# Kernel tuning notes

Hardware: AMD Instinct MI355X
Metric: run time of the kernel (lower is better)

Reference implementation:

```python
import jax, jax.numpy as jnp
import numpy as np

B, S, D, H, F, NL, V = 4, 2048, 512, 8, 2048, 4, 32000
DH = D // H
EPS = 1e-6
LN_EPS = 1e-5


def _xavier(k, shape):
    lim = (6.0 / (shape[-2] + shape[-1])) ** 0.5
    return jax.random.uniform(k, shape, jnp.float32, -lim, lim)


def setup_inputs() -> dict:
    key = jax.random.key(0)
    ks = jax.random.split(key, 12)
    x = jax.random.randint(ks[0], (B, S), 0, V)
    emb = jax.random.normal(ks[1], (V, D), jnp.float32) * 0.02
    # sinusoidal positional encoding
    pos = np.arange(S, dtype=np.float32)[:, None]
    div = np.exp(np.arange(0, D, 2, dtype=np.float32) * (-np.log(10000.0) / D))
    pe_np = np.zeros((S, D), np.float32)
    pe_np[:, 0::2] = np.sin(pos * div)
    pe_np[:, 1::2] = np.cos(pos * div)
    pe = jnp.asarray(pe_np)
    return {
        "x": x, "emb": emb, "pe": pe,
        "Wq": _xavier(ks[2], (NL, D, D)), "bq": jnp.zeros((NL, D)),
        "Wk": _xavier(ks[3], (NL, D, D)), "bk": jnp.zeros((NL, D)),
        "Wv": _xavier(ks[4], (NL, D, D)), "bv": jnp.zeros((NL, D)),
        "Wo": _xavier(ks[5], (NL, D, D)), "bo": jnp.zeros((NL, D)),
        "W1": _xavier(ks[6], (NL, D, F)), "b1": jnp.zeros((NL, F)),
        "W2": _xavier(ks[7], (NL, F, D)), "b2": jnp.zeros((NL, D)),
        "g1": jnp.ones((NL, D)), "be1": jnp.zeros((NL, D)),
        "g2": jnp.ones((NL, D)), "be2": jnp.zeros((NL, D)),
        "gf": jnp.ones((D,)), "bf": jnp.zeros((D,)),
    }


def _layer_norm(h, g, b):
    mu = jnp.mean(h, axis=-1, keepdims=True)
    var = jnp.mean((h - mu) ** 2, axis=-1, keepdims=True)
    return (h - mu) * jax.lax.rsqrt(var + LN_EPS) * g + b


def _phi(u):
    # elu(x) + 1 feature map of fast-transformers causal-linear attention
    return jax.nn.elu(u) + 1.0


def _causal_linear_attention(q, k, v, key_mask):
    # q, k, v: [B, S, H, DH]; key_mask: [B, S] (1 for valid keys)
    Q = _phi(q)
    K = _phi(k) * key_mask[:, :, None, None]
    # cumulative state sum_{j<=i} K_j outer V_j : [B, S, H, DH, DH]
    St = jnp.cumsum(K[..., :, None] * v[..., None, :], axis=1)
    num = jnp.einsum("bshd,bshde->bshe", Q, St)
    Z = 1.0 / (jnp.einsum("bshd,bshd->bsh", Q, jnp.cumsum(K, axis=1)) + EPS)
    return num * Z[..., None]


def reference(x, emb, pe, Wq, bq, Wk, bk, Wv, bv, Wo, bo,
              W1, b1, W2, b2, g1, be1, g2, be2, gf, bf):
    # length mask from nonzero token count (LengthMask semantics)
    lengths = jnp.sum(jnp.abs(x) != 0, axis=-1)  # [B]
    key_mask = (jnp.arange(S)[None, :] < lengths[:, None]).astype(jnp.float32)
    h = emb[x] + pe[None, :, :]  # [B, S, D]
    for i in range(NL):
        q = (h @ Wq[i] + bq[i]).reshape(B, S, H, DH)
        k = (h @ Wk[i] + bk[i]).reshape(B, S, H, DH)
        v = (h @ Wv[i] + bv[i]).reshape(B, S, H, DH)
        a = _causal_linear_attention(q, k, v, key_mask).reshape(B, S, D)
        a = a @ Wo[i] + bo[i]
        h = _layer_norm(h + a, g1[i], be1[i])
        y = jax.nn.relu(h @ W1[i] + b1[i]) @ W2[i] + b2[i]
        h = _layer_norm(h + y, g2[i], be2[i])
    return _layer_norm(h, gf, bf)
```

## Files before the change

kernel.cpp:

```cpp
#include <hip/hip_runtime.h>
#include <math.h>

#define NLAYER 4
#define BB 4
#define SS 2048
#define DD 512
#define HH 8
#define DH 64
#define FF 2048
#define TT (BB*SS)
#define LCH 64
#define NCH (SS/LCH)
#define LN_EPS 1e-5f
#define ATT_EPS 1e-6f

typedef __bf16 bf16x8 __attribute__((ext_vector_type(8)));
typedef float  f32x4  __attribute__((ext_vector_type(4)));

__device__ __forceinline__ unsigned short f2bf(float f) {
    union { float f; unsigned u; } a; a.f = f;
    unsigned u = a.u;
    unsigned r = (u + 0x7FFFu + ((u >> 16) & 1u)) >> 16;
    return (unsigned short)r;
}
__device__ __forceinline__ float bf2f(unsigned short s) {
    union { unsigned u; float f; } a; a.u = ((unsigned)s) << 16;
    return a.f;
}
__device__ __forceinline__ float phi_f(float u) {
    return u > 0.f ? u + 1.f : __expf(u);
}

__global__ __launch_bounds__(64)
void len_kernel(const int* __restrict__ x, int* __restrict__ len) {
    const int b = blockIdx.x;
    int cnt = 0;
    for (int s = threadIdx.x; s < SS; s += 64) cnt += (x[b * SS + s] != 0);
    #pragma unroll
    for (int off = 32; off; off >>= 1) cnt += __shfl_xor(cnt, off);
    if (threadIdx.x == 0) len[b] = cnt;
}

__global__ __launch_bounds__(256)
void embed_kernel(const int* __restrict__ x, const float* __restrict__ emb,
                  const float* __restrict__ pe, float* __restrict__ h,
                  unsigned short* __restrict__ h_bf) {
    int t = blockIdx.x * 256 + threadIdx.x;
    int row = t >> 7;
    int q = t & 127;
    int tok = x[row];
    int s = row & (SS - 1);
    float4 e = ((const float4*)(emb + (size_t)tok * DD))[q];
    float4 p = ((const float4*)(pe + (size_t)s * DD))[q];
    float4 v; v.x = e.x + p.x; v.y = e.y + p.y; v.z = e.z + p.z; v.w = e.w + p.w;
    ((float4*)(h + (size_t)row * DD))[q] = v;
    ushort4 ub; ub.x = f2bf(v.x); ub.y = f2bf(v.y); ub.z = f2bf(v.z); ub.w = f2bf(v.w);
    ((ushort4*)(h_bf + (size_t)row * DD))[q] = ub;
}

__global__ __launch_bounds__(256)
void transpose_cvt(const float* __restrict__ src, unsigned short* __restrict__ dst,
                   int R, int C, size_t srcLS, size_t dstLS) {
    __shared__ float tile[32][33];
    const int z = blockIdx.z;
    src += (size_t)z * srcLS;
    dst += (size_t)z * dstLS;
    const int c0 = blockIdx.x * 32, r0 = blockIdx.y * 32;
    const int tx = threadIdx.x & 31, ty = threadIdx.x >> 5;
    #pragma unroll
    for (int i = 0; i < 32; i += 8)
        tile[ty + i][tx] = src[(size_t)(r0 + ty + i) * C + c0 + tx];
    __syncthreads();
    #pragma unroll
    for (int i = 0; i < 32; i += 8)
        dst[(size_t)(c0 + ty + i) * R + r0 + tx] = f2bf(tile[tx][ty + i]);
}

__global__ __launch_bounds__(256)
void bias_concat(const float* __restrict__ bq, const float* __restrict__ bk,
                 const float* __restrict__ bv, float* __restrict__ bqkv) {
    int idx = blockIdx.x * 256 + threadIdx.x;
    if (idx >= NLAYER * 1536) return;
    int l = idx / 1536, n = idx % 1536;
    float v = n < 512 ? bq[l * 512 + n] : (n < 1024 ? bk[l * 512 + n - 512] : bv[l * 512 + n - 1024]);
    bqkv[idx] = v;
}

__device__ __forceinline__ void gll16(void* lds_ptr, const void* g_ptr) {
    __builtin_amdgcn_global_load_lds(
        (const __attribute__((address_space(1))) void*)g_ptr,
        (__attribute__((address_space(3))) void*)lds_ptr, 16, 0, 0);
}

template<int RELU, int WF, int WB>
__global__ __launch_bounds__(256, 2)
void gemm_bt(const unsigned short* __restrict__ A, const unsigned short* __restrict__ Bt,
             const float* __restrict__ bias, float* __restrict__ Cf,
             unsigned short* __restrict__ Cb, int M, int N, int K) {
    __shared__ __align__(16) char lds[2 * 2 * 128 * 64 * 2];
    const int Nt = N >> 7;
    const int bid = blockIdx.x;
    const int swz = (bid & 7) * ((int)gridDim.x >> 3) + (bid >> 3);
    const int m0 = (swz / Nt) * 128;
    const int n0 = (swz % Nt) * 128;
    const int tid = threadIdx.x;
    const int w = tid >> 6, lane = tid & 63;
    const int wr = w >> 1, wc = w & 1;
    const int srow = lane >> 3, scc = lane & 7;

    f32x4 acc[4][4] = {};

    auto stage = [&](int buf, int k0) {
        char* base = lds + buf * 32768;
        #pragma unroll
        for (int op = 0; op < 2; ++op) {
            const unsigned short* G = op ? Bt : A;
            const int r0 = op ? n0 : m0;
            char* obase = base + op * 16384;
            #pragma unroll
            for (int i = 0; i < 4; ++i) {
                int ii = w * 4 + i;
                int row = ii * 8 + srow;
                int chunk = scc ^ (row & 7);
                gll16(obase + ii * 1024,
                      G + (size_t)(r0 + row) * K + k0 + chunk * 8);
            }
        }
    };

    stage(0, 0);
    const int nt = K >> 6;
    int buf = 0;
    const int g = lane >> 4;
    const int rA = wr * 64 + (lane & 15);
    const int rB = wc * 64 + (lane & 15);

    for (int kt = 0; kt < nt; ++kt) {
        __syncthreads();
        if (kt + 1 < nt) stage(buf ^ 1, (kt + 1) << 6);
        const char* pA = lds + buf * 32768;
        const char* pB = pA + 16384;
        bf16x8 af[4][2], bfr[4][2];
        #pragma unroll
        for (int m = 0; m < 4; ++m)
            #pragma unroll
            for (int kk = 0; kk < 2; ++kk) {
                int row = rA + m * 16;
                int c = (kk * 4 + g) ^ (row & 7);
                af[m][kk] = *(const bf16x8*)(pA + row * 128 + c * 16);
            }
        #pragma unroll
        for (int n = 0; n < 4; ++n)
            #pragma unroll
            for (int kk = 0; kk < 2; ++kk) {
                int row = rB + n * 16;
                int c = (kk * 4 + g) ^ (row & 7);
                bfr[n][kk] = *(const bf16x8*)(pB + row * 128 + c * 16);
            }
        #pragma unroll
        for (int kk = 0; kk < 2; ++kk)
            #pragma unroll
            for (int m = 0; m < 4; ++m)
                #pragma unroll
                for (int n = 0; n < 4; ++n)
                    acc[m][n] = __builtin_amdgcn_mfma_f32_16x16x32_bf16(
                        af[m][kk], bfr[n][kk], acc[m][n], 0, 0, 0);
        buf ^= 1;
    }

    const int col16 = lane & 15;
    const int rgrp = lane >> 4;
    #pragma unroll
    for (int n = 0; n < 4; ++n) {
        int col = n0 + wc * 64 + n * 16 + col16;
        float bi = bias[col];
        #pragma unroll
        for (int m = 0; m < 4; ++m) {
            int rowb = m0 + wr * 64 + m * 16 + rgrp * 4;
            #pragma unroll
            for (int r = 0; r < 4; ++r) {
                float v = acc[m][n][r] + bi;
                if (RELU) v = v > 0.f ? v : 0.f;
                if (WF) Cf[(size_t)(rowb + r) * N + col] = v;
                if (WB) Cb[(size_t)(rowb + r) * N + col] = f2bf(v);
            }
        }
    }
}

__global__ __launch_bounds__(256)
void attn_chunk_sums(const unsigned short* __restrict__ qkv, const int* __restrict__ len,
                     unsigned short* __restrict__ states, float* __restrict__ ksum) {
    const int c = blockIdx.x & (NCH - 1);
    const int bh = blockIdx.x / NCH;
    const int b = bh >> 3, h = bh & 7;
    const int L = len[b];
    const int tid = threadIdx.x;
    const int w = tid >> 6, lane = tid & 63;
    __shared__ __align__(16) unsigned short Kt[64 * 64];
    __shared__ __align__(16) unsigned short Vt[64 * 64];
    __shared__ float ksumP[4][64];

    float kpart = 0.f;
    #pragma unroll 8
    for (int t = 0; t < 16; ++t) {
        const int jj = 4 * t + w;
        const int d = lane;
        const int sglob = c * 64 + jj;
        const unsigned short* base = qkv + (size_t)(b * SS + sglob) * 1536 + h * 64 + d;
        float kv = bf2f(base[512]);
        float kp = (sglob < L) ? phi_f(kv) : 0.f;
        kpart += kp;
        const int sw = (((jj >> 3) ^ (d & 7)) << 3) + (jj & 7);
        Kt[d * 64 + sw] = f2bf(kp);
        Vt[d * 64 + sw] = base[1024];
    }
    ksumP[w][lane] = kpart;
    __syncthreads();

    const int frow = w * 16 + (lane & 15);
    const int g = lane >> 4;
    bf16x8 ak[2];
    #pragma unroll
    for (int kk = 0; kk < 2; ++kk)
        ak[kk] = *(const bf16x8*)&Kt[frow * 64 + (((kk * 4 + g) ^ (frow & 7)) << 3)];
    f32x4 oc[4] = {};
    #pragma unroll
    for (int ef = 0; ef < 4; ++ef) {
        int brow = ef * 16 + (lane & 15);
        #pragma unroll
        for (int kk = 0; kk < 2; ++kk) {
            bf16x8 bv = *(const bf16x8*)&Vt[brow * 64 + (((kk * 4 + g) ^ (brow & 7)) << 3)];
            oc[ef] = __builtin_amdgcn_mfma_f32_16x16x32_bf16(ak[kk], bv, oc[ef], 0, 0, 0);
        }
    }
    unsigned short* so = states + (size_t)blockIdx.x * 4096;
    #pragma unroll
    for (int ef = 0; ef < 4; ++ef)
        #pragma unroll
        for (int r = 0; r < 4; ++r) {
            int dd = w * 16 + g * 4 + r;
            int e = ef * 16 + (lane & 15);
            so[dd * 64 + e] = f2bf(oc[ef][r]);
        }
    if (w == 0) {
        float s = ksumP[0][lane] + ksumP[1][lane] + ksumP[2][lane] + ksumP[3][lane];
        ksum[(size_t)blockIdx.x * 64 + lane] = s;
    }
}

__global__ __launch_bounds__(256)
void attn_prefix(const unsigned short* __restrict__ states, const float* __restrict__ ksum,
                 unsigned short* __restrict__ sprefix, float* __restrict__ kprefix) {
    const int bh = blockIdx.x >> 4;
    const int idx = (blockIdx.x & 15) * 256 + threadIdx.x;
    size_t base = (size_t)bh * NCH * 4096 + idx;
    float run = 0.f;
    #pragma unroll 4
    for (int cc = 0; cc < NCH; ++cc) {
        size_t o = base + (size_t)cc * 4096;
        float v = bf2f(states[o]);
        sprefix[o] = f2bf(run);
        run += v;
    }
    if ((blockIdx.x & 15) == 0 && threadIdx.x < 64) {
        size_t kb = (size_t)bh * NCH * 64 + threadIdx.x;
        float krun = 0.f;
        for (int cc = 0; cc < NCH; ++cc) {
            size_t o = kb + (size_t)cc * 64;
            float v = ksum[o];
            kprefix[o] = krun;
            krun += v;
        }
    }
}

__global__ __launch_bounds__(256)
void attn_output(const unsigned short* __restrict__ qkv, const int* __restrict__ len,
                 const unsigned short* __restrict__ sprefix, const float* __restrict__ kprefix,
                 unsigned short* __restrict__ a_bf) {
    const int c = blockIdx.x & (NCH - 1);
    const int bh = blockIdx.x / NCH;
    const int b = bh >> 3, h = bh & 7;
    const int L = len[b];
    const int tid = threadIdx.x;
    const int w = tid >> 6, lane = tid & 63;

    __shared__ __align__(16) unsigned short Qb[64 * 64];
    __shared__ __align__(16) unsigned short Kb[64 * 64];
    __shared__ __align__(16) unsigned short SpT[64 * 64];
    __shared__ __align__(16) unsigned short Vt[64 * 64];
    __shared__ __align__(16) unsigned short Amb[64 * 64];
    __shared__ float zq[64];
    __shared__ float zinv[64];

    const float kspv = kprefix[(size_t)(bh * NCH + c) * 64 + lane];
    const unsigned short* Sp = sprefix + (size_t)(bh * NCH + c) * 4096;

    #pragma unroll 4
    for (int t = 0; t < 16; ++t) {
        const int jj = 4 * t + w;
        const int d = lane;
        const int sglob = c * 64 + jj;
        const unsigned short* base = qkv + (size_t)(b * SS + sglob) * 1536 + h * 64 + d;
        float qv = bf2f(base[0]), kv = bf2f(base[512]);
        float qp = phi_f(qv);
        float kp = (sglob < L) ? phi_f(kv) : 0.f;
        const int swr = (((d >> 3) ^ (jj & 7)) << 3) + (d & 7);
        Qb[jj * 64 + swr] = f2bf(qp);
        Kb[jj * 64 + swr] = f2bf(kp);
        const int swt = (((jj >> 3) ^ (d & 7)) << 3) + (jj & 7);
        Vt[d * 64 + swt] = base[1024];
        SpT[d * 64 + swt] = Sp[jj * 64 + d];
        float zc = qp * kspv;
        #pragma unroll
        for (int off = 32; off; off >>= 1) zc += __shfl_xor(zc, off);
        if (lane == 0) zq[jj] = zc;
    }
    __syncthreads();

    const int frow = w * 16 + (lane & 15);
    const int g = lane >> 4;
    bf16x8 aq[2];
    #pragma unroll
    for (int kk = 0; kk < 2; ++kk)
        aq[kk] = *(const bf16x8*)&Qb[frow * 64 + (((kk * 4 + g) ^ (frow & 7)) << 3)];

    f32x4 am[4] = {};
    #pragma unroll
    for (int jf = 0; jf < 4; ++jf) {
        int brow = jf * 16 + (lane & 15);
        #pragma unroll
        for (int kk = 0; kk < 2; ++kk) {
            bf16x8 bk = *(const bf16x8*)&Kb[brow * 64 + (((kk * 4 + g) ^ (brow & 7)) << 3)];
            am[jf] = __builtin_amdgcn_mfma_f32_16x16x32_bf16(aq[kk], bk, am[jf], 0, 0, 0);
        }
    }

    float zl[4] = {0.f, 0.f, 0.f, 0.f};
    #pragma unroll
    for (int jf = 0; jf < 4; ++jf) {
        #pragma unroll
        for (int r = 0; r < 4; ++r) {
            int i = w * 16 + g * 4 + r;
            int j = jf * 16 + (lane & 15);
            float v = (j <= i) ? am[jf][r] : 0.f;
            zl[r] += v;
            Amb[i * 64 + (((j >> 3) ^ (i & 7)) << 3) + (j & 7)] = f2bf(v);
        }
    }
    #pragma unroll
    for (int r = 0; r < 4; ++r)
        #pragma unroll
        for (int off = 1; off < 16; off <<= 1) zl[r] += __shfl_xor(zl[r], off);
    #pragma unroll
    for (int r = 0; r < 4; ++r) {
        if ((lane & 15) == r) {
            int i = w * 16 + g * 4 + r;
            zinv[i] = 1.f / (zl[r] + zq[i] + ATT_EPS);
        }
    }

    f32x4 oc[4] = {};
    #pragma unroll
    for (int ef = 0; ef < 4; ++ef) {
        int brow = ef * 16 + (lane & 15);
        #pragma unroll
        for (int kk = 0; kk < 2; ++kk) {
            bf16x8 bs = *(const bf16x8*)&SpT[brow * 64 + (((kk * 4 + g) ^ (brow & 7)) << 3)];
            oc[ef] = __builtin_amdgcn_mfma_f32_16x16x32_bf16(aq[kk], bs, oc[ef], 0, 0, 0);
        }
    }
    bf16x8 aam[2];
    #pragma unroll
    for (int kk = 0; kk < 2; ++kk)
        aam[kk] = *(const bf16x8*)&Amb[frow * 64 + (((kk * 4 + g) ^ (frow & 7)) << 3)];
    #pragma unroll
    for (int ef = 0; ef < 4; ++ef) {
        int brow = ef * 16 + (lane & 15);
        #pragma unroll
        for (int kk = 0; kk < 2; ++kk) {
            bf16x8 bv = *(const bf16x8*)&Vt[brow * 64 + (((kk * 4 + g) ^ (brow & 7)) << 3)];
            oc[ef] = __builtin_amdgcn_mfma_f32_16x16x32_bf16(aam[kk], bv, oc[ef], 0, 0, 0);
        }
    }

    __syncthreads();
    #pragma unroll
    for (int ef = 0; ef < 4; ++ef) {
        #pragma unroll
        for (int r = 0; r < 4; ++r) {
            int i = w * 16 + g * 4 + r;
            int e = ef * 16 + (lane & 15);
            float zi = zinv[i];
            Kb[i * 64 + (((e >> 3) ^ (i & 7)) << 3) + (e & 7)] = f2bf(oc[ef][r] * zi);
        }
    }
    __syncthreads();
    {
        unsigned short* dst = a_bf + (size_t)(b * SS + c * 64) * 512 + h * 64;
        #pragma unroll
        for (int u = 0; u < 2; ++u) {
            int cid = tid + u * 256;
            int row = cid >> 3, cb = cid & 7;
            int4 val = *(const int4*)&Kb[row * 64 + ((cb ^ (row & 7)) << 3)];
            *(int4*)(dst + (size_t)row * 512 + cb * 8) = val;
        }
    }
}

template<int ADD, int WB>
__global__ __launch_bounds__(64)
void ln_kernel(const float* __restrict__ hin, const float* __restrict__ add,
               const float* __restrict__ gw, const float* __restrict__ bw,
               float* __restrict__ hout, unsigned short* __restrict__ hbf) {
    const int row = blockIdx.x;
    const int lane = threadIdx.x;
    float v[8];
    const float* hp = hin + (size_t)row * DD;
    float s = 0.f;
    #pragma unroll
    for (int i = 0; i < 2; ++i) {
        int q = lane + i * 64;
        float4 a = ((const float4*)hp)[q];
        if (ADD) {
            float4 bb = ((const float4*)(add + (size_t)row * DD))[q];
            a.x += bb.x; a.y += bb.y; a.z += bb.z; a.w += bb.w;
        }
        v[i*4+0] = a.x; v[i*4+1] = a.y; v[i*4+2] = a.z; v[i*4+3] = a.w;
        s += a.x + a.y + a.z + a.w;
    }
    #pragma unroll
    for (int off = 32; off; off >>= 1) s += __shfl_xor(s, off);
    float mu = s * (1.f / 512.f);
    float sq = 0.f;
    #pragma unroll
    for (int i = 0; i < 8; ++i) { float d = v[i] - mu; sq += d * d; }
    #pragma unroll
    for (int off = 32; off; off >>= 1) sq += __shfl_xor(sq, off);
    float rs = 1.f / sqrtf(sq * (1.f / 512.f) + LN_EPS);
    #pragma unroll
    for (int i = 0; i < 2; ++i) {
        int q = lane + i * 64;
        float4 gv = ((const float4*)gw)[q];
        float4 bv = ((const float4*)bw)[q];
        float4 o;
        o.x = (v[i*4+0] - mu) * rs * gv.x + bv.x;
        o.y = (v[i*4+1] - mu) * rs * gv.y + bv.y;
        o.z = (v[i*4+2] - mu) * rs * gv.z + bv.z;
        o.w = (v[i*4+3] - mu) * rs * gv.w + bv.w;
        ((float4*)(hout + (size_t)row * DD))[q] = o;
        if (WB) {
            ushort4 ub; ub.x = f2bf(o.x); ub.y = f2bf(o.y); ub.z = f2bf(o.z); ub.w = f2bf(o.w);
            ((ushort4*)(hbf + (size_t)row * DD))[q] = ub;
        }
    }
}

extern "C" void kernel_launch(void* const* d_in, const int* in_sizes, int n_in,
                              void* d_out, int out_size, void* d_ws, size_t ws_size,
                              hipStream_t stream) {
    (void)in_sizes; (void)n_in; (void)out_size; (void)ws_size;
    const int*   x   = (const int*)d_in[0];
    const float* emb = (const float*)d_in[1];
    const float* pe  = (const float*)d_in[2];
    const float* Wq  = (const float*)d_in[3];
    const float* bq  = (const float*)d_in[4];
    const float* Wk  = (const float*)d_in[5];
    const float* bk  = (const float*)d_in[6];
    const float* Wv  = (const float*)d_in[7];
    const float* bv  = (const float*)d_in[8];
    const float* Wo  = (const float*)d_in[9];
    const float* bo  = (const float*)d_in[10];
    const float* W1  = (const float*)d_in[11];
    const float* b1  = (const float*)d_in[12];
    const float* W2  = (const float*)d_in[13];
    const float* b2  = (const float*)d_in[14];
    const float* g1  = (const float*)d_in[15];
    const float* be1 = (const float*)d_in[16];
    const float* g2  = (const float*)d_in[17];
    const float* be2 = (const float*)d_in[18];
    const float* gf  = (const float*)d_in[19];
    const float* bff = (const float*)d_in[20];
    float* out = (float*)d_out;

    char* ws = (char*)d_ws;
    size_t off = 0;
    auto alloc = [&](size_t bytes) -> void* {
        void* p = ws + off; off += (bytes + 255) & ~(size_t)255; return p;
    };
    int* len              = (int*)alloc(16);
    unsigned short* qkv_t = (unsigned short*)alloc((size_t)NLAYER * 1536 * 512 * 2);
    unsigned short* wo_t  = (unsigned short*)alloc((size_t)NLAYER * 512 * 512 * 2);
    unsigned short* w1_t  = (unsigned short*)alloc((size_t)NLAYER * 2048 * 512 * 2);
    unsigned short* w2_t  = (unsigned short*)alloc((size_t)NLAYER * 512 * 2048 * 2);
    float* bqkv           = (float*)alloc((size_t)NLAYER * 1536 * 4);
    float* h              = (float*)alloc((size_t)TT * 512 * 4);
    unsigned short* h_bf  = (unsigned short*)alloc((size_t)TT * 512 * 2);
    unsigned short* qkv   = (unsigned short*)alloc((size_t)TT * 1536 * 2);
    unsigned short* a_bf  = (unsigned short*)alloc((size_t)TT * 512 * 2);
    float* obuf           = (float*)alloc((size_t)TT * 512 * 4);
    unsigned short* y1_bf = (unsigned short*)alloc((size_t)TT * 2048 * 2);
    unsigned short* states  = (unsigned short*)alloc((size_t)32 * NCH * 4096 * 2);
    float* ksum           = (float*)alloc((size_t)32 * NCH * 64 * 4);
    unsigned short* sprefix = (unsigned short*)alloc((size_t)32 * NCH * 4096 * 2);
    float* kprefix        = (float*)alloc((size_t)32 * NCH * 64 * 4);

    len_kernel<<<BB, 64, 0, stream>>>(x, len);
    embed_kernel<<<(TT * 128) / 256, 256, 0, stream>>>(x, emb, pe, h, h_bf);

    dim3 tb(256);
    transpose_cvt<<<dim3(16, 16, NLAYER), tb, 0, stream>>>(Wq, qkv_t,             512, 512, (size_t)512*512, (size_t)1536*512);
    transpose_cvt<<<dim3(16, 16, NLAYER), tb, 0, stream>>>(Wk, qkv_t + 512*512,   512, 512, (size_t)512*512, (size_t)1536*512);
    transpose_cvt<<<dim3(16, 16, NLAYER), tb, 0, stream>>>(Wv, qkv_t + 1024*512,  512, 512, (size_t)512*512, (size_t)1536*512);
    transpose_cvt<<<dim3(16, 16, NLAYER), tb, 0, stream>>>(Wo, wo_t,              512, 512, (size_t)512*512, (size_t)512*512);
    transpose_cvt<<<dim3(64, 16, NLAYER), tb, 0, stream>>>(W1, w1_t,              512, 2048, (size_t)512*2048, (size_t)2048*512);
    transpose_cvt<<<dim3(16, 64, NLAYER), tb, 0, stream>>>(W2, w2_t,              2048, 512, (size_t)2048*512, (size_t)512*2048);
    bias_concat<<<(NLAYER * 1536 + 255) / 256, 256, 0, stream>>>(bq, bk, bv, bqkv);

    for (int l = 0; l < NLAYER; ++l) {
        gemm_bt<0,0,1><<<(TT/128) * (1536/128), 256, 0, stream>>>(
            h_bf, qkv_t + (size_t)l*1536*512, bqkv + l*1536, nullptr, qkv, TT, 1536, 512);
        attn_chunk_sums<<<32 * NCH, 256, 0, stream>>>(qkv, len, states, ksum);
        attn_prefix<<<32 * 16, 256, 0, stream>>>(states, ksum, sprefix, kprefix);
        attn_output<<<32 * NCH, 256, 0, stream>>>(qkv, len, sprefix, kprefix, a_bf);
        gemm_bt<0,1,0><<<(TT/128) * (512/128), 256, 0, stream>>>(
            a_bf, wo_t + (size_t)l*512*512, bo + l*512, obuf, nullptr, TT, 512, 512);
        ln_kernel<1,1><<<TT, 64, 0, stream>>>(h, obuf, g1 + l*512, be1 + l*512, h, h_bf);
        gemm_bt<1,0,1><<<(TT/128) * (2048/128), 256, 0, stream>>>(
            h_bf, w1_t + (size_t)l*2048*512, b1 + l*2048, nullptr, y1_bf, TT, 2048, 512);
        gemm_bt<0,1,0><<<(TT/128) * (512/128), 256, 0, stream>>>(
            y1_bf, w2_t + (size_t)l*512*2048, b2 + l*512, obuf, nullptr, TT, 512, 2048);
        ln_kernel<1,1><<<TT, 64, 0, stream>>>(h, obuf, g2 + l*512, be2 + l*512, h, h_bf);
    }
    ln_kernel<0,0><<<TT, 64, 0, stream>>>(h, nullptr, gf, bff, out, nullptr);
}
```

Baseline: 594.5 us.

## Add 256x256-tile 8-wave GEMM with interleaved prefetch for QKV and FFN1

Adds a new GEMM kernel using 256x256 output tiles, 512 threads, 128KB of double-buffered LDS with XOR swizzle, and staging of the next K tile interleaved between MFMA phases with setprio and a grid swizzle. It replaces the 128x128 GEMM for the QKV projection and the first FFN matmul. The goal is more reuse per loaded tile and better overlap of global loads with MFMA work. In exchange, grids get smaller (192 and 256 blocks), which may leave CUs underfilled, and the large LDS footprint limits occupancy.

```diff
diff --git a/kernel.cpp b/kernel.cpp
--- a/kernel.cpp
+++ b/kernel.cpp
@@ -177,6 +177,111 @@
         #pragma unroll
         for (int m = 0; m < 4; ++m) {
             int rowb = m0 + wr * 64 + m * 16 + rgrp * 4;
+            #pragma unroll
+            for (int r = 0; r < 4; ++r) {
+                float v = acc[m][n][r] + bi;
+                if (RELU) v = v > 0.f ? v : 0.f;
+                if (WF) Cf[(size_t)(rowb + r) * N + col] = v;
+                if (WB) Cb[(size_t)(rowb + r) * N + col] = f2bf(v);
+            }
+        }
+    }
+}
+
+template<int RELU, int WF, int WB>
+__global__ __launch_bounds__(512, 2)
+void gemm8p(const unsigned short* __restrict__ A, const unsigned short* __restrict__ Bt,
+            const float* __restrict__ bias, float* __restrict__ Cf,
+            unsigned short* __restrict__ Cb, int M, int N, int K) {
+    __shared__ __align__(16) char lds[131072];
+    const int Nt = N >> 8;
+    const int bid = blockIdx.x;
+    const int swz = (bid & 7) * ((int)gridDim.x >> 3) + (bid >> 3);
+    const int m0 = (swz / Nt) * 256;
+    const int n0 = (swz % Nt) * 256;
+    const int tid = threadIdx.x;
+    const int w = tid >> 6, lane = tid & 63;
+    const int wr = w >> 2, wc = w & 3;
+    const int srow = lane >> 3, scc = lane & 7;
+    const int g = lane >> 4, l16 = lane & 15;
+
+    f32x4 acc[8][4] = {};
+
+    auto stageA = [&](int buf, int k0) {
+        char* base = lds + buf * 65536;
+        #pragma unroll
+        for (int i = 0; i < 4; ++i) {
+            int ii = w * 4 + i;
+            int row = ii * 8 + srow;
+            int chunk = scc ^ (row & 7);
+            gll16(base + ii * 1024, A + (size_t)(m0 + row) * K + k0 + chunk * 8);
+        }
+    };
+    auto stageB = [&](int buf, int k0) {
+        char* base = lds + buf * 65536 + 32768;
+        #pragma unroll
+        for (int i = 0; i < 4; ++i) {
+            int ii = w * 4 + i;
+            int row = ii * 8 + srow;
+            int chunk = scc ^ (row & 7);
+            gll16(base + ii * 1024, Bt + (size_t)(n0 + row) * K + k0 + chunk * 8);
+        }
+    };
+
+    stageA(0, 0); stageB(0, 0);
+    asm volatile("s_waitcnt vmcnt(0)" ::: "memory");
+    __builtin_amdgcn_s_barrier();
+    __builtin_amdgcn_sched_barrier(0);
+
+    const int nt = K >> 6;
+    for (int t = 0; t < nt; ++t) {
+        const int bufc = t & 1;
+        const char* pA = lds + bufc * 65536;
+        const char* pB = pA + 32768;
+        bf16x8 bfr[4][2];
+        #pragma unroll
+        for (int n = 0; n < 4; ++n)
+            #pragma unroll
+            for (int kk = 0; kk < 2; ++kk) {
+                int row = wc * 64 + n * 16 + l16;
+                bfr[n][kk] = *(const bf16x8*)(pB + row * 128 + (((kk * 4 + g) ^ (row & 7)) << 4));
+            }
+        #pragma unroll
+        for (int p = 0; p < 4; ++p) {
+            bf16x8 af[2][2];
+            #pragma unroll
+            for (int mi = 0; mi < 2; ++mi)
+                #pragma unroll
+                for (int kk = 0; kk < 2; ++kk) {
+                    int row = wr * 128 + (p * 2 + mi) * 16 + l16;
+                    af[mi][kk] = *(const bf16x8*)(pA + row * 128 + (((kk * 4 + g) ^ (row & 7)) << 4));
+                }
+            if (p == 0 && t + 1 < nt) stageA(bufc ^ 1, (t + 1) << 6);
+            if (p == 1 && t + 1 < nt) stageB(bufc ^ 1, (t + 1) << 6);
+            __builtin_amdgcn_s_barrier();
+            __builtin_amdgcn_s_setprio(1);
+            #pragma unroll
+            for (int kk = 0; kk < 2; ++kk)
+                #pragma unroll
+                for (int mi = 0; mi < 2; ++mi)
+                    #pragma unroll
+                    for (int n = 0; n < 4; ++n)
+                        acc[p * 2 + mi][n] = __builtin_amdgcn_mfma_f32_16x16x32_bf16(
+                            af[mi][kk], bfr[n][kk], acc[p * 2 + mi][n], 0, 0, 0);
+            __builtin_amdgcn_s_setprio(0);
+            if (p == 3) asm volatile("s_waitcnt vmcnt(0)" ::: "memory");
+            __builtin_amdgcn_s_barrier();
+            __builtin_amdgcn_sched_barrier(0);
+        }
+    }
+
+    #pragma unroll
+    for (int n = 0; n < 4; ++n) {
+        int col = n0 + wc * 64 + n * 16 + l16;
+        float bi = bias[col];
+        #pragma unroll
+        for (int m = 0; m < 8; ++m) {
+            int rowb = m0 + wr * 128 + m * 16 + g * 4;
             #pragma unroll
             for (int r = 0; r < 4; ++r) {
                 float v = acc[m][n][r] + bi;
@@ -519,7 +624,7 @@
     bias_concat<<<(NLAYER * 1536 + 255) / 256, 256, 0, stream>>>(bq, bk, bv, bqkv);
 
     for (int l = 0; l < NLAYER; ++l) {
-        gemm_bt<0,0,1><<<(TT/128) * (1536/128), 256, 0, stream>>>(
+        gemm8p<0,0,1><<<(TT/256) * (1536/256), 512, 0, stream>>>(
             h_bf, qkv_t + (size_t)l*1536*512, bqkv + l*1536, nullptr, qkv, TT, 1536, 512);
         attn_chunk_sums<<<32 * NCH, 256, 0, stream>>>(qkv, len, states, ksum);
         attn_prefix<<<32 * 16, 256, 0, stream>>>(states, ksum, sprefix, kprefix);
@@ -527,7 +632,7 @@
         gemm_bt<0,1,0><<<(TT/128) * (512/128), 256, 0, stream>>>(
             a_bf, wo_t + (size_t)l*512*512, bo + l*512, obuf, nullptr, TT, 512, 512);
         ln_kernel<1,1><<<TT, 64, 0, stream>>>(h, obuf, g1 + l*512, be1 + l*512, h, h_bf);
-        gemm_bt<1,0,1><<<(TT/128) * (2048/128), 256, 0, stream>>>(
+        gemm8p<1,0,1><<<(TT/256) * (2048/256), 512, 0, stream>>>(
             h_bf, w1_t + (size_t)l*2048*512, b1 + l*2048, nullptr, y1_bf, TT, 2048, 512);
         gemm_bt<0,1,0><<<(TT/128) * (512/128), 256, 0, stream>>>(
             y1_bf, w2_t + (size_t)l*512*2048, b2 + l*512, obuf, nullptr, TT, 512, 2048);
```

Measured after the change: 642.2 us. 1.08x slower.
